# Performance work log

Measured on AMD Instinct MI355X. Metric: run time of the kernel, lower is better.

Reference implementation:

```python
import jax, jax.numpy as jnp
import numpy as np

B, F, A, U = 4096, 64, 8, 32  # batch, n_features, num_att, n_outputs
R = 2.0                       # the 'r' scaling inside exp(kernel * r)


def setup_inputs() -> dict:
    key = jax.random.key(0)
    k1, k2 = jax.random.split(key)
    inputs = jax.random.normal(k1, (B, F), dtype=jnp.float32)
    # per-exclusion-feature attention kernels, stacked: [F, A, F, U]
    limit = float(np.sqrt(6.0 / (F + U)))  # glorot_uniform
    kernels = jax.random.uniform(k2, (F, A, F, U), dtype=jnp.float32,
                                 minval=-limit, maxval=limit)
    return {"inputs": inputs, "kernels": kernels}


def reference(inputs, kernels):
    # inputs: [B, F]; kernels: [j=F excluded-feature index, A, F, U]
    f = inputs.shape[-1]
    mask = 1.0 - jnp.eye(f, dtype=inputs.dtype)          # [j, F]: zero out feature j
    xm = mask[:, None, :] * inputs[None, :, :]           # [j, B, F]
    z = jnp.einsum('jbf,jafu->jabu', xm, kernels)        # [j, A, B, U]
    z = jax.nn.softmax(z, axis=-1)                       # softmax over units
    w = jnp.exp(kernels * R)                             # [j, A, F, U]
    scores = jnp.einsum('jabu,jafu->jabf', z, w)         # [j, A, B, F]
    scores = scores.mean(axis=0)                         # mean over exclusion axis -> [A, B, F]
    return jax.nn.softmax(scores, axis=-1)               # [A, B, F]
```

## Files before the change

kernel.cpp:

```cpp
#include <hip/hip_runtime.h>
#include <hip/hip_bf16.h>
#include <math.h>

#define B_ 4096
#define F_ 64
#define A_ 8
#define U_ 32

typedef float f32x4 __attribute__((ext_vector_type(4)));
typedef short bf16x8 __attribute__((ext_vector_type(8)));

#define KD_OFF (4ull << 20)

static __device__ __forceinline__ unsigned int pk_bf16(float lo, float hi) {
    union { __hip_bfloat162 h2; unsigned int u; } cv;
    cv.h2 = __float22bfloat162_rn(make_float2(lo, hi));
    return cv.u;
}
static __device__ __forceinline__ float rb(float f) {
    unsigned int u = __float_as_uint(f);
    u += 0x7FFFu + ((u >> 16) & 1u);
    return __uint_as_float(u & 0xFFFF0000u);
}

__global__ __launch_bounds__(256) void ife_prep(const float* __restrict__ kern,
                                                unsigned char* __restrict__ ws)
{
    const int bid = blockIdx.x;
    const int a = bid >> 6, j = bid & 63;
    const int t = threadIdx.x;
    __shared__ float st[64][36];

    const float* src = kern + ((size_t)j * A_ + a) * (F_ * U_);
    {
        const int f = t >> 2, u0 = (t & 3) * 8;
        *(float4*)&st[f][u0]     = *(const float4*)&src[f * U_ + u0];
        *(float4*)&st[f][u0 + 4] = *(const float4*)&src[f * U_ + u0 + 4];
    }
    __syncthreads();

    unsigned char* dst = ws + (size_t)bid * 8192;
    const int fragid = t >> 6, lane = t & 63, q = lane >> 4, c = lane & 15;

    {
        const int kc = fragid >> 1, ut = fragid & 1;
        const int f0 = kc * 32 + q * 8, u = ut * 16 + c;
        unsigned int w[4];
        #pragma unroll
        for (int i = 0; i < 4; ++i)
            w[i] = pk_bf16(st[f0 + 2 * i][u], st[f0 + 2 * i + 1][u]);
        *(uint4*)(dst + fragid * 1024 + lane * 16) = make_uint4(w[0], w[1], w[2], w[3]);
    }
    {
        const int f = fragid * 16 + c, u0 = q * 8;
        const float4 wa = *(const float4*)&st[f][u0];
        const float4 wb = *(const float4*)&st[f][u0 + 4];
        unsigned int w[4];
        w[0] = pk_bf16(__expf(2.f * wa.x), __expf(2.f * wa.y));
        w[1] = pk_bf16(__expf(2.f * wa.z), __expf(2.f * wa.w));
        w[2] = pk_bf16(__expf(2.f * wb.x), __expf(2.f * wb.y));
        w[3] = pk_bf16(__expf(2.f * wb.z), __expf(2.f * wb.w));
        *(uint4*)(dst + 4096 + fragid * 1024 + lane * 16) = make_uint4(w[0], w[1], w[2], w[3]);
    }
    if (t < U_)
        ((float*)(ws + KD_OFF))[(size_t)bid * U_ + t] = rb(st[j][t]);
}

__global__ __launch_bounds__(256, 2) void ife_main(const float* __restrict__ x,
                                                   const unsigned char* __restrict__ ws,
                                                   float* __restrict__ out)
{
    const int a = blockIdx.y, bt = blockIdx.x, t = threadIdx.x;
    const int wv = t >> 6, lane = t & 63, q = lane >> 4, c = lane & 15;

    __shared__ float Xf[64][66];
    __shared__ float Kd[64][32];
    __shared__ __align__(16) unsigned int Pbuf[4][16][20];

    bf16x8 Xh[2];
    {
        const float* xr = x + (size_t)(bt * 64 + wv * 16 + c) * F_;
        #pragma unroll
        for (int kc = 0; kc < 2; ++kc) {
            const float4 va = *(const float4*)&xr[kc * 32 + q * 8];
            const float4 vb = *(const float4*)&xr[kc * 32 + q * 8 + 4];
            union { unsigned int u[4]; bf16x8 v; } H;
            H.u[0] = pk_bf16(va.x, va.y);
            H.u[1] = pk_bf16(va.z, va.w);
            H.u[2] = pk_bf16(vb.x, vb.y);
            H.u[3] = pk_bf16(vb.z, vb.w);
            Xh[kc] = H.v;
        }
    }
    {
        const int row = t >> 2, cb = (t & 3) * 16;
        const float* xsrc = x + (size_t)(bt * 64 + row) * F_ + cb;
        #pragma unroll
        for (int i = 0; i < 16; i += 4) {
            const float4 v = *(const float4*)&xsrc[i];
            Xf[row][cb + i]     = rb(v.x);
            Xf[row][cb + i + 1] = rb(v.y);
            Xf[row][cb + i + 2] = rb(v.z);
            Xf[row][cb + i + 3] = rb(v.w);
        }
    }
    {
        const float* kd = (const float*)(ws + KD_OFF) + (size_t)a * 64 * U_;
        const int jj = t >> 2, u0 = (t & 3) * 8;
        *(float4*)&Kd[jj][u0]     = *(const float4*)&kd[jj * U_ + u0];
        *(float4*)&Kd[jj][u0 + 4] = *(const float4*)&kd[jj * U_ + u0 + 4];
    }
    __syncthreads();

    const unsigned int psel = (q < 2) ? 0x05040100u : 0x07060302u;
    const unsigned char* fbase = ws + (size_t)a * 64 * 8192 + (size_t)lane * 16;

    union { unsigned int u[4]; bf16x8 v; } oc;
    oc.u[0] = 0x3F803F80u; oc.u[1] = 0x3F803F80u; oc.u[2] = 0x3F803F80u; oc.u[3] = 0x3F803F80u;
    const bf16x8 ONES = oc.v;
    const f32x4 vzero = (f32x4){0.f, 0.f, 0.f, 0.f};

    f32x4 S0 = vzero, S1 = vzero, S2 = vzero, S3 = vzero;

    bf16x8 KA[4], WA[4], KB[4], WB[4];

    auto LOADF = [&](bf16x8* K, bf16x8* W, int jj) {
        const unsigned char* p = fbase + (size_t)jj * 8192;
        #pragma unroll
        for (int i = 0; i < 4; ++i) {
            K[i] = *(const bf16x8*)(p + i * 1024);
            W[i] = *(const bf16x8*)(p + 4096 + i * 1024);
        }
    };

    auto BODY = [&](const bf16x8* K, const bf16x8* W, int j) {
        f32x4 ZA = vzero, ZB = vzero;
        ZA = __builtin_amdgcn_mfma_f32_16x16x32_bf16(Xh[0], K[0], ZA, 0, 0, 0);
        ZA = __builtin_amdgcn_mfma_f32_16x16x32_bf16(Xh[1], K[2], ZA, 0, 0, 0);
        ZB = __builtin_amdgcn_mfma_f32_16x16x32_bf16(Xh[0], K[1], ZB, 0, 0, 0);
        ZB = __builtin_amdgcn_mfma_f32_16x16x32_bf16(Xh[1], K[3], ZB, 0, 0, 0);

        const float kd0 = Kd[j][c], kd1 = Kd[j][16 + c];
        #pragma unroll
        for (int r = 0; r < 4; ++r) {
            const float xj = Xf[wv * 16 + q * 4 + r][j];
            const float e0 = __expf(ZA[r] - xj * kd0);
            const float e1 = __expf(ZB[r] - xj * kd1);
            Pbuf[wv][q * 4 + r][c] = pk_bf16(e0, e1);
        }
        asm volatile("s_waitcnt lgkmcnt(0)" ::: "memory");
        union { unsigned int u[4]; bf16x8 v; } E;
        {
            const uint4 pa = *(const uint4*)&Pbuf[wv][c][(q & 1) * 8];
            const uint4 pb = *(const uint4*)&Pbuf[wv][c][(q & 1) * 8 + 4];
            E.u[0] = __builtin_amdgcn_perm(pa.y, pa.x, psel);
            E.u[1] = __builtin_amdgcn_perm(pa.w, pa.z, psel);
            E.u[2] = __builtin_amdgcn_perm(pb.y, pb.x, psel);
            E.u[3] = __builtin_amdgcn_perm(pb.w, pb.z, psel);
        }

        const f32x4 sv = __builtin_amdgcn_mfma_f32_16x16x32_bf16(E.v, ONES, vzero, 0, 0, 0);
        f32x4 D0 = __builtin_amdgcn_mfma_f32_16x16x32_bf16(E.v, W[0], vzero, 0, 0, 0);
        f32x4 D1 = __builtin_amdgcn_mfma_f32_16x16x32_bf16(E.v, W[1], vzero, 0, 0, 0);
        f32x4 D2 = __builtin_amdgcn_mfma_f32_16x16x32_bf16(E.v, W[2], vzero, 0, 0, 0);
        f32x4 D3 = __builtin_amdgcn_mfma_f32_16x16x32_bf16(E.v, W[3], vzero, 0, 0, 0);
        #pragma unroll
        for (int r = 0; r < 4; ++r) {
            const float inv = __builtin_amdgcn_rcpf(sv[r]);
            S0[r] += D0[r] * inv;
            S1[r] += D1[r] * inv;
            S2[r] += D2[r] * inv;
            S3[r] += D3[r] * inv;
        }
    };

    LOADF(KA, WA, 0);
    for (int j = 0; j < 64; j += 2) {
        LOADF(KB, WB, j + 1);
        BODY(KA, WA, j);
        LOADF(KA, WA, (j + 2 < 64) ? (j + 2) : 63);
        BODY(KB, WB, j + 1);
    }

    const float sc = 1.f / 64.f;
    #pragma unroll
    for (int r = 0; r < 4; ++r) {
        const float e0 = __expf(S0[r] * sc);
        const float e1 = __expf(S1[r] * sc);
        const float e2 = __expf(S2[r] * sc);
        const float e3 = __expf(S3[r] * sc);
        float s = e0 + e1 + e2 + e3;
        s += __shfl_xor(s, 1);
        s += __shfl_xor(s, 2);
        s += __shfl_xor(s, 4);
        s += __shfl_xor(s, 8);
        const float inv = 1.f / s;
        const int b = bt * 64 + wv * 16 + q * 4 + r;
        float* o = out + ((size_t)a * B_ + b) * F_ + c;
        o[0]  = e0 * inv;
        o[16] = e1 * inv;
        o[32] = e2 * inv;
        o[48] = e3 * inv;
    }
}

extern "C" void kernel_launch(void* const* d_in, const int* in_sizes, int n_in,
                              void* d_out, int out_size, void* d_ws, size_t ws_size,
                              hipStream_t stream) {
    (void)in_sizes; (void)n_in; (void)out_size; (void)ws_size;
    const float* x    = (const float*)d_in[0];
    const float* kern = (const float*)d_in[1];
    float* out        = (float*)d_out;
    unsigned char* ws = (unsigned char*)d_ws;

    hipLaunchKernelGGL(ife_prep, dim3(F_ * A_), dim3(256), 0, stream, kern, ws);
    hipLaunchKernelGGL(ife_main, dim3(B_ / 64, A_), dim3(256), 0, stream, x, ws, out);
}
```

Before: 98.16 us.

## Fuse prep and main into persistent kernel with grid barriers and split-j reduction

Replaces the two launches with one persistent 512-block kernel. Each block first does the weight prep, waits at a software grid barrier, then computes half of the exclusion axis for 128 batch rows. Partial sums from the two halves are exchanged through workspace (one half stored as bf16) and combined after a second barrier before the final softmax. This removes a launch and doubles row reuse of each loaded weight fragment, but it relies on all 512 blocks being co-resident, adds barrier spin cost and a memset, and rounds one partial sum to bf16.

```diff
diff --git a/kernel.cpp b/kernel.cpp
--- a/kernel.cpp
+++ b/kernel.cpp
@@ -10,17 +10,272 @@
 typedef float f32x4 __attribute__((ext_vector_type(4)));
 typedef short bf16x8 __attribute__((ext_vector_type(8)));
 
-#define KD_OFF (4ull << 20)
+#define KD_OFF   (4ull << 20)
+#define PART_OFF ((4ull << 20) + (64ull << 10))
+#define BAR_OFF  (PART_OFF + (4ull << 20))
+#define WS_NEED  (BAR_OFF + 128ull)
 
 static __device__ __forceinline__ unsigned int pk_bf16(float lo, float hi) {
     union { __hip_bfloat162 h2; unsigned int u; } cv;
     cv.h2 = __float22bfloat162_rn(make_float2(lo, hi));
     return cv.u;
 }
+static __device__ __forceinline__ unsigned short rne16(float f) {
+    unsigned int u = __float_as_uint(f);
+    u += 0x7FFFu + ((u >> 16) & 1u);
+    return (unsigned short)(u >> 16);
+}
 static __device__ __forceinline__ float rb(float f) {
     unsigned int u = __float_as_uint(f);
     u += 0x7FFFu + ((u >> 16) & 1u);
     return __uint_as_float(u & 0xFFFF0000u);
+}
+static __device__ __forceinline__ float b2f(unsigned short h) {
+    return __uint_as_float(((unsigned int)h) << 16);
+}
+
+static __device__ __forceinline__ void grid_barrier(unsigned int* bar, unsigned int target) {
+    __threadfence();
+    __syncthreads();
+    if (threadIdx.x == 0) {
+        __hip_atomic_fetch_add(bar, 1u, __ATOMIC_ACQ_REL, __HIP_MEMORY_SCOPE_AGENT);
+        while (__hip_atomic_load(bar, __ATOMIC_RELAXED, __HIP_MEMORY_SCOPE_AGENT) < target)
+            __builtin_amdgcn_s_sleep(1);
+    }
+    __syncthreads();
+    __threadfence();
+}
+
+__global__ __launch_bounds__(256, 2)
+void ife_fused(const float* __restrict__ x,
+               const float* __restrict__ kern,
+               unsigned char* __restrict__ ws,
+               float* __restrict__ out)
+{
+    const int b = blockIdx.x, t = threadIdx.x;
+    const int wv = t >> 6, lane = t & 63, q = lane >> 4, c = lane & 15;
+    unsigned int* bar = (unsigned int*)(ws + BAR_OFF);
+
+    __shared__ union {
+        float st[64][36];
+        struct {
+            float Xf[128][33];
+            float Kd[32][32];
+            unsigned int Pbuf[4][2][16][20];
+        } p2;
+    } sh;
+
+    {
+        const int ap = b >> 6, jp = b & 63;
+        const float* src = kern + ((size_t)jp * A_ + ap) * (F_ * U_);
+        {
+            const int f = t >> 2, u0 = (t & 3) * 8;
+            *(float4*)&sh.st[f][u0]     = *(const float4*)&src[f * U_ + u0];
+            *(float4*)&sh.st[f][u0 + 4] = *(const float4*)&src[f * U_ + u0 + 4];
+        }
+        __syncthreads();
+        unsigned char* dst = ws + (size_t)b * 8192;
+        const int fragid = t >> 6;
+        {
+            const int kc = fragid >> 1, ut = fragid & 1;
+            const int f0 = kc * 32 + q * 8, u = ut * 16 + c;
+            unsigned int w[4];
+            #pragma unroll
+            for (int i = 0; i < 4; ++i)
+                w[i] = pk_bf16(sh.st[f0 + 2 * i][u], sh.st[f0 + 2 * i + 1][u]);
+            *(uint4*)(dst + fragid * 1024 + lane * 16) = make_uint4(w[0], w[1], w[2], w[3]);
+        }
+        {
+            const int ff = fragid * 16 + c, u0 = q * 8;
+            const float4 wa = *(const float4*)&sh.st[ff][u0];
+            const float4 wb = *(const float4*)&sh.st[ff][u0 + 4];
+            unsigned int w[4];
+            w[0] = pk_bf16(__expf(2.f * wa.x), __expf(2.f * wa.y));
+            w[1] = pk_bf16(__expf(2.f * wa.z), __expf(2.f * wa.w));
+            w[2] = pk_bf16(__expf(2.f * wb.x), __expf(2.f * wb.y));
+            w[3] = pk_bf16(__expf(2.f * wb.z), __expf(2.f * wb.w));
+            *(uint4*)(dst + 4096 + fragid * 1024 + lane * 16) = make_uint4(w[0], w[1], w[2], w[3]);
+        }
+        if (t < U_)
+            ((float*)(ws + KD_OFF))[(size_t)b * U_ + t] = rb(sh.st[b & 63][t]);
+    }
+    grid_barrier(bar, 512u);
+
+    const int a = b >> 6, bt = (b >> 1) & 31, h = b & 1;
+    const int R0 = bt * 128;
+
+    bf16x8 Xh[2][2];
+    #pragma unroll
+    for (int rg = 0; rg < 2; ++rg) {
+        const float* xr = x + (size_t)(R0 + wv * 32 + rg * 16 + c) * F_;
+        #pragma unroll
+        for (int kc = 0; kc < 2; ++kc) {
+            const float4 va = *(const float4*)&xr[kc * 32 + q * 8];
+            const float4 vb = *(const float4*)&xr[kc * 32 + q * 8 + 4];
+            union { unsigned int u[4]; bf16x8 v; } H;
+            H.u[0] = pk_bf16(va.x, va.y);
+            H.u[1] = pk_bf16(va.z, va.w);
+            H.u[2] = pk_bf16(vb.x, vb.y);
+            H.u[3] = pk_bf16(vb.z, vb.w);
+            Xh[rg][kc] = H.v;
+        }
+    }
+    {
+        const int row = t >> 1, cs = (t & 1) * 16;
+        const float* xsrc = x + (size_t)(R0 + row) * F_ + h * 32 + cs;
+        #pragma unroll
+        for (int i = 0; i < 16; i += 4) {
+            const float4 v = *(const float4*)&xsrc[i];
+            sh.p2.Xf[row][cs + i]     = rb(v.x);
+            sh.p2.Xf[row][cs + i + 1] = rb(v.y);
+            sh.p2.Xf[row][cs + i + 2] = rb(v.z);
+            sh.p2.Xf[row][cs + i + 3] = rb(v.w);
+        }
+    }
+    {
+        const int jl = t >> 3, u0 = (t & 7) * 4;
+        const float* kd = (const float*)(ws + KD_OFF) + ((size_t)(a * 64 + h * 32 + jl)) * U_ + u0;
+        *(float4*)&sh.p2.Kd[jl][u0] = *(const float4*)kd;
+    }
+    __syncthreads();
+
+    const unsigned int psel = (q < 2) ? 0x05040100u : 0x07060302u;
+    const unsigned char* fbase = ws + (size_t)(a * 64 + h * 32) * 8192 + (size_t)lane * 16;
+
+    union { unsigned int u[4]; bf16x8 v; } oc;
+    oc.u[0] = 0x3F803F80u; oc.u[1] = 0x3F803F80u; oc.u[2] = 0x3F803F80u; oc.u[3] = 0x3F803F80u;
+    const bf16x8 ONES = oc.v;
+    const f32x4 vzero = (f32x4){0.f, 0.f, 0.f, 0.f};
+
+    f32x4 S[2][4];
+    #pragma unroll
+    for (int rg = 0; rg < 2; ++rg)
+        #pragma unroll
+        for (int ft = 0; ft < 4; ++ft) S[rg][ft] = vzero;
+
+    bf16x8 KA[4], WA[4], KB[4], WB[4];
+    auto LOADF = [&](bf16x8* K, bf16x8* W, int jl) {
+        const unsigned char* p = fbase + (size_t)jl * 8192;
+        #pragma unroll
+        for (int i = 0; i < 4; ++i) {
+            K[i] = *(const bf16x8*)(p + i * 1024);
+            W[i] = *(const bf16x8*)(p + 4096 + i * 1024);
+        }
+    };
+
+    auto BODY = [&](const bf16x8* K, const bf16x8* W, int jl) {
+        f32x4 ZA[2], ZB[2];
+        #pragma unroll
+        for (int rg = 0; rg < 2; ++rg) {
+            f32x4 za = vzero, zb = vzero;
+            za = __builtin_amdgcn_mfma_f32_16x16x32_bf16(Xh[rg][0], K[0], za, 0, 0, 0);
+            za = __builtin_amdgcn_mfma_f32_16x16x32_bf16(Xh[rg][1], K[2], za, 0, 0, 0);
+            zb = __builtin_amdgcn_mfma_f32_16x16x32_bf16(Xh[rg][0], K[1], zb, 0, 0, 0);
+            zb = __builtin_amdgcn_mfma_f32_16x16x32_bf16(Xh[rg][1], K[3], zb, 0, 0, 0);
+            ZA[rg] = za; ZB[rg] = zb;
+        }
+        const float kd0 = sh.p2.Kd[jl][c], kd1 = sh.p2.Kd[jl][16 + c];
+        #pragma unroll
+        for (int rg = 0; rg < 2; ++rg)
+            #pragma unroll
+            for (int r = 0; r < 4; ++r) {
+                const float xj = sh.p2.Xf[wv * 32 + rg * 16 + q * 4 + r][jl];
+                const float e0 = __expf(ZA[rg][r] - xj * kd0);
+                const float e1 = __expf(ZB[rg][r] - xj * kd1);
+                sh.p2.Pbuf[wv][rg][q * 4 + r][c] = pk_bf16(e0, e1);
+            }
+        asm volatile("s_waitcnt lgkmcnt(0)" ::: "memory");
+        union { unsigned int u[4]; bf16x8 v; } E[2];
+        #pragma unroll
+        for (int rg = 0; rg < 2; ++rg) {
+            const uint4 pa = *(const uint4*)&sh.p2.Pbuf[wv][rg][c][(q & 1) * 8];
+            const uint4 pb = *(const uint4*)&sh.p2.Pbuf[wv][rg][c][(q & 1) * 8 + 4];
+            E[rg].u[0] = __builtin_amdgcn_perm(pa.y, pa.x, psel);
+            E[rg].u[1] = __builtin_amdgcn_perm(pa.w, pa.z, psel);
+            E[rg].u[2] = __builtin_amdgcn_perm(pb.y, pb.x, psel);
+            E[rg].u[3] = __builtin_amdgcn_perm(pb.w, pb.z, psel);
+        }
+        #pragma unroll
+        for (int rg = 0; rg < 2; ++rg) {
+            const f32x4 sv = __builtin_amdgcn_mfma_f32_16x16x32_bf16(E[rg].v, ONES, vzero, 0, 0, 0);
+            f32x4 D[4];
+            #pragma unroll
+            for (int ft = 0; ft < 4; ++ft)
+                D[ft] = __builtin_amdgcn_mfma_f32_16x16x32_bf16(E[rg].v, W[ft], vzero, 0, 0, 0);
+            #pragma unroll
+            for (int r = 0; r < 4; ++r) {
+                const float inv = __builtin_amdgcn_rcpf(sv[r]);
+                #pragma unroll
+                for (int ft = 0; ft < 4; ++ft) S[rg][ft][r] += D[ft][r] * inv;
+            }
+        }
+    };
+
+    LOADF(KA, WA, 0);
+    for (int jl = 0; jl < 32; jl += 2) {
+        LOADF(KB, WB, jl + 1);
+        BODY(KA, WA, jl);
+        LOADF(KA, WA, (jl + 2 < 32) ? (jl + 2) : 31);
+        BODY(KB, WB, jl + 1);
+    }
+
+    {
+        const float sc = 1.f / 64.f;
+        if (h == 0) {
+            unsigned short* part = (unsigned short*)(ws + PART_OFF);
+            #pragma unroll
+            for (int rg = 0; rg < 2; ++rg)
+                #pragma unroll
+                for (int r = 0; r < 4; ++r) {
+                    const int row = R0 + wv * 32 + rg * 16 + q * 4 + r;
+                    unsigned short* p = part + ((size_t)a * 4096 + row) * 64 + c;
+                    p[0]  = rne16(S[rg][0][r] * sc);
+                    p[16] = rne16(S[rg][1][r] * sc);
+                    p[32] = rne16(S[rg][2][r] * sc);
+                    p[48] = rne16(S[rg][3][r] * sc);
+                }
+        } else {
+            #pragma unroll
+            for (int rg = 0; rg < 2; ++rg)
+                #pragma unroll
+                for (int r = 0; r < 4; ++r) {
+                    const int row = R0 + wv * 32 + rg * 16 + q * 4 + r;
+                    float* p = out + ((size_t)a * B_ + row) * F_ + c;
+                    p[0]  = S[rg][0][r] * sc;
+                    p[16] = S[rg][1][r] * sc;
+                    p[32] = S[rg][2][r] * sc;
+                    p[48] = S[rg][3][r] * sc;
+                }
+        }
+    }
+    grid_barrier(bar, 1024u);
+
+    {
+        const unsigned short* part = (const unsigned short*)(ws + PART_OFF);
+        const int Row0 = bt * 128 + h * 64;
+        #pragma unroll
+        for (int r = 0; r < 4; ++r) {
+            const int row = Row0 + wv * 16 + q * 4 + r;
+            const unsigned short* P0 = part + ((size_t)a * 4096 + row) * 64 + c;
+            float* o = out + ((size_t)a * B_ + row) * F_ + c;
+            const float v0 = b2f(P0[0])  + o[0];
+            const float v1 = b2f(P0[16]) + o[16];
+            const float v2 = b2f(P0[32]) + o[32];
+            const float v3 = b2f(P0[48]) + o[48];
+            const float e0 = __expf(v0), e1 = __expf(v1);
+            const float e2 = __expf(v2), e3 = __expf(v3);
+            float s = e0 + e1 + e2 + e3;
+            s += __shfl_xor(s, 1);
+            s += __shfl_xor(s, 2);
+            s += __shfl_xor(s, 4);
+            s += __shfl_xor(s, 8);
+            const float inv = 1.f / s;
+            o[0]  = e0 * inv;
+            o[16] = e1 * inv;
+            o[32] = e2 * inv;
+            o[48] = e3 * inv;
+        }
+    }
 }
 
 __global__ __launch_bounds__(256) void ife_prep(const float* __restrict__ kern,
@@ -30,7 +285,6 @@
     const int a = bid >> 6, j = bid & 63;
     const int t = threadIdx.x;
     __shared__ float st[64][36];
-
     const float* src = kern + ((size_t)j * A_ + a) * (F_ * U_);
     {
         const int f = t >> 2, u0 = (t & 3) * 8;
@@ -38,10 +292,8 @@
         *(float4*)&st[f][u0 + 4] = *(const float4*)&src[f * U_ + u0 + 4];
     }
     __syncthreads();
-
     unsigned char* dst = ws + (size_t)bid * 8192;
     const int fragid = t >> 6, lane = t & 63, q = lane >> 4, c = lane & 15;
-
     {
         const int kc = fragid >> 1, ut = fragid & 1;
         const int f0 = kc * 32 + q * 8, u = ut * 16 + c;
@@ -52,9 +304,9 @@
         *(uint4*)(dst + fragid * 1024 + lane * 16) = make_uint4(w[0], w[1], w[2], w[3]);
     }
     {
-        const int f = fragid * 16 + c, u0 = q * 8;
-        const float4 wa = *(const float4*)&st[f][u0];
-        const float4 wb = *(const float4*)&st[f][u0 + 4];
+        const int ff = fragid * 16 + c, u0 = q * 8;
+        const float4 wa = *(const float4*)&st[ff][u0];
+        const float4 wb = *(const float4*)&st[ff][u0 + 4];
         unsigned int w[4];
         w[0] = pk_bf16(__expf(2.f * wa.x), __expf(2.f * wa.y));
         w[1] = pk_bf16(__expf(2.f * wa.z), __expf(2.f * wa.w));
@@ -72,7 +324,6 @@
 {
     const int a = blockIdx.y, bt = blockIdx.x, t = threadIdx.x;
     const int wv = t >> 6, lane = t & 63, q = lane >> 4, c = lane & 15;
-
     __shared__ float Xf[64][66];
     __shared__ float Kd[64][32];
     __shared__ __align__(16) unsigned int Pbuf[4][16][20];
@@ -114,14 +365,11 @@
 
     const unsigned int psel = (q < 2) ? 0x05040100u : 0x07060302u;
     const unsigned char* fbase = ws + (size_t)a * 64 * 8192 + (size_t)lane * 16;
-
     union { unsigned int u[4]; bf16x8 v; } oc;
     oc.u[0] = 0x3F803F80u; oc.u[1] = 0x3F803F80u; oc.u[2] = 0x3F803F80u; oc.u[3] = 0x3F803F80u;
     const bf16x8 ONES = oc.v;
     const f32x4 vzero = (f32x4){0.f, 0.f, 0.f, 0.f};
-
     f32x4 S0 = vzero, S1 = vzero, S2 = vzero, S3 = vzero;
-
     bf16x8 KA[4], WA[4], KB[4], WB[4];
 
     auto LOADF = [&](bf16x8* K, bf16x8* W, int jj) {
@@ -132,14 +380,12 @@
             W[i] = *(const bf16x8*)(p + 4096 + i * 1024);
         }
     };
-
     auto BODY = [&](const bf16x8* K, const bf16x8* W, int j) {
         f32x4 ZA = vzero, ZB = vzero;
         ZA = __builtin_amdgcn_mfma_f32_16x16x32_bf16(Xh[0], K[0], ZA, 0, 0, 0);
         ZA = __builtin_amdgcn_mfma_f32_16x16x32_bf16(Xh[1], K[2], ZA, 0, 0, 0);
         ZB = __builtin_amdgcn_mfma_f32_16x16x32_bf16(Xh[0], K[1], ZB, 0, 0, 0);
         ZB = __builtin_amdgcn_mfma_f32_16x16x32_bf16(Xh[1], K[3], ZB, 0, 0, 0);
-
         const float kd0 = Kd[j][c], kd1 = Kd[j][16 + c];
         #pragma unroll
         for (int r = 0; r < 4; ++r) {
@@ -158,7 +404,6 @@
             E.u[2] = __builtin_amdgcn_perm(pb.y, pb.x, psel);
             E.u[3] = __builtin_amdgcn_perm(pb.w, pb.z, psel);
         }
-
         const f32x4 sv = __builtin_amdgcn_mfma_f32_16x16x32_bf16(E.v, ONES, vzero, 0, 0, 0);
         f32x4 D0 = __builtin_amdgcn_mfma_f32_16x16x32_bf16(E.v, W[0], vzero, 0, 0, 0);
         f32x4 D1 = __builtin_amdgcn_mfma_f32_16x16x32_bf16(E.v, W[1], vzero, 0, 0, 0);
@@ -181,7 +426,6 @@
         LOADF(KA, WA, (j + 2 < 64) ? (j + 2) : 63);
         BODY(KB, WB, j + 1);
     }
-
     const float sc = 1.f / 64.f;
     #pragma unroll
     for (int r = 0; r < 4; ++r) {
@@ -195,8 +439,8 @@
         s += __shfl_xor(s, 4);
         s += __shfl_xor(s, 8);
         const float inv = 1.f / s;
-        const int b = bt * 64 + wv * 16 + q * 4 + r;
-        float* o = out + ((size_t)a * B_ + b) * F_ + c;
+        const int bb = bt * 64 + wv * 16 + q * 4 + r;
+        float* o = out + ((size_t)a * B_ + bb) * F_ + c;
         o[0]  = e0 * inv;
         o[16] = e1 * inv;
         o[32] = e2 * inv;
@@ -207,12 +451,17 @@
 extern "C" void kernel_launch(void* const* d_in, const int* in_sizes, int n_in,
                               void* d_out, int out_size, void* d_ws, size_t ws_size,
                               hipStream_t stream) {
-    (void)in_sizes; (void)n_in; (void)out_size; (void)ws_size;
+    (void)in_sizes; (void)n_in; (void)out_size;
     const float* x    = (const float*)d_in[0];
     const float* kern = (const float*)d_in[1];
     float* out        = (float*)d_out;
     unsigned char* ws = (unsigned char*)d_ws;
 
-    hipLaunchKernelGGL(ife_prep, dim3(F_ * A_), dim3(256), 0, stream, kern, ws);
-    hipLaunchKernelGGL(ife_main, dim3(B_ / 64, A_), dim3(256), 0, stream, x, ws, out);
-}
+    if (ws_size >= WS_NEED) {
+        hipMemsetAsync(ws + BAR_OFF, 0, 128, stream);
+        hipLaunchKernelGGL(ife_fused, dim3(512), dim3(256), 0, stream, x, kern, ws, out);
+    } else {
+        hipLaunchKernelGGL(ife_prep, dim3(F_ * A_), dim3(256), 0, stream, kern, ws);
+        hipLaunchKernelGGL(ife_main, dim3(B_ / 64, A_), dim3(256), 0, stream, x, ws, out);
+    }
+}
```

Measured after the change: 344.4 us. 251% more time.

## Fuse kernel preprocessing into main kernel with double-buffered LDS fragments

Applied to the files above, without the earlier changes.

Removes the separate prep kernel that converted kernels to bf16 MFMA fragments and exp-weights in a workspace. Each main block now loads raw fp32 kernel slices per exclusion index, converts them and writes them into double-buffered LDS. This saves a launch and the workspace round trip. In exchange, every block recomputes the conversion and exp work (redundant across 64 batch tiles), and a block-wide barrier is added on every iteration.

```diff
diff --git a/kernel.cpp b/kernel.cpp
--- a/kernel.cpp
+++ b/kernel.cpp
@@ -10,8 +10,6 @@
 typedef float f32x4 __attribute__((ext_vector_type(4)));
 typedef short bf16x8 __attribute__((ext_vector_type(8)));
 
-#define KD_OFF (4ull << 20)
-
 static __device__ __forceinline__ unsigned int pk_bf16(float lo, float hi) {
     union { __hip_bfloat162 h2; unsigned int u; } cv;
     cv.h2 = __float22bfloat162_rn(make_float2(lo, hi));
@@ -23,59 +21,18 @@
     return __uint_as_float(u & 0xFFFF0000u);
 }
 
-__global__ __launch_bounds__(256) void ife_prep(const float* __restrict__ kern,
-                                                unsigned char* __restrict__ ws)
-{
-    const int bid = blockIdx.x;
-    const int a = bid >> 6, j = bid & 63;
-    const int t = threadIdx.x;
-    __shared__ float st[64][36];
-
-    const float* src = kern + ((size_t)j * A_ + a) * (F_ * U_);
-    {
-        const int f = t >> 2, u0 = (t & 3) * 8;
-        *(float4*)&st[f][u0]     = *(const float4*)&src[f * U_ + u0];
-        *(float4*)&st[f][u0 + 4] = *(const float4*)&src[f * U_ + u0 + 4];
-    }
-    __syncthreads();
-
-    unsigned char* dst = ws + (size_t)bid * 8192;
-    const int fragid = t >> 6, lane = t & 63, q = lane >> 4, c = lane & 15;
-
-    {
-        const int kc = fragid >> 1, ut = fragid & 1;
-        const int f0 = kc * 32 + q * 8, u = ut * 16 + c;
-        unsigned int w[4];
-        #pragma unroll
-        for (int i = 0; i < 4; ++i)
-            w[i] = pk_bf16(st[f0 + 2 * i][u], st[f0 + 2 * i + 1][u]);
-        *(uint4*)(dst + fragid * 1024 + lane * 16) = make_uint4(w[0], w[1], w[2], w[3]);
-    }
-    {
-        const int f = fragid * 16 + c, u0 = q * 8;
-        const float4 wa = *(const float4*)&st[f][u0];
-        const float4 wb = *(const float4*)&st[f][u0 + 4];
-        unsigned int w[4];
-        w[0] = pk_bf16(__expf(2.f * wa.x), __expf(2.f * wa.y));
-        w[1] = pk_bf16(__expf(2.f * wa.z), __expf(2.f * wa.w));
-        w[2] = pk_bf16(__expf(2.f * wb.x), __expf(2.f * wb.y));
-        w[3] = pk_bf16(__expf(2.f * wb.z), __expf(2.f * wb.w));
-        *(uint4*)(dst + 4096 + fragid * 1024 + lane * 16) = make_uint4(w[0], w[1], w[2], w[3]);
-    }
-    if (t < U_)
-        ((float*)(ws + KD_OFF))[(size_t)bid * U_ + t] = rb(st[j][t]);
-}
-
-__global__ __launch_bounds__(256, 2) void ife_main(const float* __restrict__ x,
-                                                   const unsigned char* __restrict__ ws,
-                                                   float* __restrict__ out)
+__global__ __launch_bounds__(256, 2)
+void ife_onepass(const float* __restrict__ x,
+                 const float* __restrict__ kern,
+                 float* __restrict__ out)
 {
     const int a = blockIdx.y, bt = blockIdx.x, t = threadIdx.x;
     const int wv = t >> 6, lane = t & 63, q = lane >> 4, c = lane & 15;
 
     __shared__ float Xf[64][66];
-    __shared__ float Kd[64][32];
     __shared__ __align__(16) unsigned int Pbuf[4][16][20];
+    __shared__ __align__(16) uint4 Kfr[2][4][64];
+    __shared__ __align__(16) uint4 Wfr[2][4][64];
 
     bf16x8 Xh[2];
     {
@@ -104,43 +61,65 @@
             Xf[row][cb + i + 3] = rb(v.w);
         }
     }
-    {
-        const float* kd = (const float*)(ws + KD_OFF) + (size_t)a * 64 * U_;
-        const int jj = t >> 2, u0 = (t & 3) * 8;
-        *(float4*)&Kd[jj][u0]     = *(const float4*)&kd[jj * U_ + u0];
-        *(float4*)&Kd[jj][u0 + 4] = *(const float4*)&kd[jj * U_ + u0 + 4];
-    }
+
+    const int kcP = wv >> 1, utP = wv & 1;
+
+    float4 w0, w1; float kr[8]; float2 kdn;
+    auto PREP_LOAD = [&](int jn) {
+        const float* kj = kern + ((size_t)jn * A_ + a) * (F_ * U_);
+        const float* wrow = kj + (wv * 16 + c) * U_ + q * 8;
+        w0 = *(const float4*)wrow;
+        w1 = *(const float4*)(wrow + 4);
+        const float* kcol = kj + (kcP * 32 + q * 8) * U_ + utP * 16 + c;
+        #pragma unroll
+        for (int i = 0; i < 8; ++i) kr[i] = kcol[i * U_];
+        kdn.x = kj[jn * U_ + c];
+        kdn.y = kj[jn * U_ + 16 + c];
+    };
+    auto PREP_STORE = [&](int pb) {
+        uint4 kw, ww;
+        kw.x = pk_bf16(kr[0], kr[1]);
+        kw.y = pk_bf16(kr[2], kr[3]);
+        kw.z = pk_bf16(kr[4], kr[5]);
+        kw.w = pk_bf16(kr[6], kr[7]);
+        ww.x = pk_bf16(__expf(2.f * w0.x), __expf(2.f * w0.y));
+        ww.y = pk_bf16(__expf(2.f * w0.z), __expf(2.f * w0.w));
+        ww.z = pk_bf16(__expf(2.f * w1.x), __expf(2.f * w1.y));
+        ww.w = pk_bf16(__expf(2.f * w1.z), __expf(2.f * w1.w));
+        Kfr[pb][wv][lane] = kw;
+        Wfr[pb][wv][lane] = ww;
+    };
+
+    PREP_LOAD(0);
+    PREP_STORE(0);
+    float2 kdc = kdn;
     __syncthreads();
 
     const unsigned int psel = (q < 2) ? 0x05040100u : 0x07060302u;
-    const unsigned char* fbase = ws + (size_t)a * 64 * 8192 + (size_t)lane * 16;
-
     union { unsigned int u[4]; bf16x8 v; } oc;
     oc.u[0] = 0x3F803F80u; oc.u[1] = 0x3F803F80u; oc.u[2] = 0x3F803F80u; oc.u[3] = 0x3F803F80u;
     const bf16x8 ONES = oc.v;
     const f32x4 vzero = (f32x4){0.f, 0.f, 0.f, 0.f};
-
     f32x4 S0 = vzero, S1 = vzero, S2 = vzero, S3 = vzero;
 
-    bf16x8 KA[4], WA[4], KB[4], WB[4];
+    for (int j = 0; j < 64; ++j) {
+        const int buf = j & 1;
+        PREP_LOAD((j + 1 < 64) ? (j + 1) : 63);
 
-    auto LOADF = [&](bf16x8* K, bf16x8* W, int jj) {
-        const unsigned char* p = fbase + (size_t)jj * 8192;
+        union { uint4 u; bf16x8 v; } K[4], W[4];
         #pragma unroll
         for (int i = 0; i < 4; ++i) {
-            K[i] = *(const bf16x8*)(p + i * 1024);
-            W[i] = *(const bf16x8*)(p + 4096 + i * 1024);
+            K[i].u = Kfr[buf][i][lane];
+            W[i].u = Wfr[buf][i][lane];
         }
-    };
 
-    auto BODY = [&](const bf16x8* K, const bf16x8* W, int j) {
         f32x4 ZA = vzero, ZB = vzero;
-        ZA = __builtin_amdgcn_mfma_f32_16x16x32_bf16(Xh[0], K[0], ZA, 0, 0, 0);
-        ZA = __builtin_amdgcn_mfma_f32_16x16x32_bf16(Xh[1], K[2], ZA, 0, 0, 0);
-        ZB = __builtin_amdgcn_mfma_f32_16x16x32_bf16(Xh[0], K[1], ZB, 0, 0, 0);
-        ZB = __builtin_amdgcn_mfma_f32_16x16x32_bf16(Xh[1], K[3], ZB, 0, 0, 0);
+        ZA = __builtin_amdgcn_mfma_f32_16x16x32_bf16(Xh[0], K[0].v, ZA, 0, 0, 0);
+        ZA = __builtin_amdgcn_mfma_f32_16x16x32_bf16(Xh[1], K[2].v, ZA, 0, 0, 0);
+        ZB = __builtin_amdgcn_mfma_f32_16x16x32_bf16(Xh[0], K[1].v, ZB, 0, 0, 0);
+        ZB = __builtin_amdgcn_mfma_f32_16x16x32_bf16(Xh[1], K[3].v, ZB, 0, 0, 0);
 
-        const float kd0 = Kd[j][c], kd1 = Kd[j][16 + c];
+        const float kd0 = rb(kdc.x), kd1 = rb(kdc.y);
         #pragma unroll
         for (int r = 0; r < 4; ++r) {
             const float xj = Xf[wv * 16 + q * 4 + r][j];
@@ -160,10 +139,10 @@
         }
 
         const f32x4 sv = __builtin_amdgcn_mfma_f32_16x16x32_bf16(E.v, ONES, vzero, 0, 0, 0);
-        f32x4 D0 = __builtin_amdgcn_mfma_f32_16x16x32_bf16(E.v, W[0], vzero, 0, 0, 0);
-        f32x4 D1 = __builtin_amdgcn_mfma_f32_16x16x32_bf16(E.v, W[1], vzero, 0, 0, 0);
-        f32x4 D2 = __builtin_amdgcn_mfma_f32_16x16x32_bf16(E.v, W[2], vzero, 0, 0, 0);
-        f32x4 D3 = __builtin_amdgcn_mfma_f32_16x16x32_bf16(E.v, W[3], vzero, 0, 0, 0);
+        f32x4 D0 = __builtin_amdgcn_mfma_f32_16x16x32_bf16(E.v, W[0].v, vzero, 0, 0, 0);
+        f32x4 D1 = __builtin_amdgcn_mfma_f32_16x16x32_bf16(E.v, W[1].v, vzero, 0, 0, 0);
+        f32x4 D2 = __builtin_amdgcn_mfma_f32_16x16x32_bf16(E.v, W[2].v, vzero, 0, 0, 0);
+        f32x4 D3 = __builtin_amdgcn_mfma_f32_16x16x32_bf16(E.v, W[3].v, vzero, 0, 0, 0);
         #pragma unroll
         for (int r = 0; r < 4; ++r) {
             const float inv = __builtin_amdgcn_rcpf(sv[r]);
@@ -172,14 +151,10 @@
             S2[r] += D2[r] * inv;
             S3[r] += D3[r] * inv;
         }
-    };
 
-    LOADF(KA, WA, 0);
-    for (int j = 0; j < 64; j += 2) {
-        LOADF(KB, WB, j + 1);
-        BODY(KA, WA, j);
-        LOADF(KA, WA, (j + 2 < 64) ? (j + 2) : 63);
-        BODY(KB, WB, j + 1);
+        PREP_STORE(buf ^ 1);
+        __syncthreads();
+        kdc = kdn;
     }
 
     const float sc = 1.f / 64.f;
@@ -195,8 +170,8 @@
         s += __shfl_xor(s, 4);
         s += __shfl_xor(s, 8);
         const float inv = 1.f / s;
-        const int b = bt * 64 + wv * 16 + q * 4 + r;
-        float* o = out + ((size_t)a * B_ + b) * F_ + c;
+        const int bb = bt * 64 + wv * 16 + q * 4 + r;
+        float* o = out + ((size_t)a * B_ + bb) * F_ + c;
         o[0]  = e0 * inv;
         o[16] = e1 * inv;
         o[32] = e2 * inv;
@@ -207,12 +182,10 @@
 extern "C" void kernel_launch(void* const* d_in, const int* in_sizes, int n_in,
                               void* d_out, int out_size, void* d_ws, size_t ws_size,
                               hipStream_t stream) {
-    (void)in_sizes; (void)n_in; (void)out_size; (void)ws_size;
+    (void)in_sizes; (void)n_in; (void)out_size; (void)d_ws; (void)ws_size;
     const float* x    = (const float*)d_in[0];
     const float* kern = (const float*)d_in[1];
     float* out        = (float*)d_out;
-    unsigned char* ws = (unsigned char*)d_ws;
 
-    hipLaunchKernelGGL(ife_prep, dim3(F_ * A_), dim3(256), 0, stream, kern, ws);
-    hipLaunchKernelGGL(ife_main, dim3(B_ / 64, A_), dim3(256), 0, stream, x, ws, out);
+    hipLaunchKernelGGL(ife_onepass, dim3(B_ / 64, A_), dim3(256), 0, stream, x, kern, out);
 }
```

Result: slower. 122.3 us (+24.6%).
